# Kernel optimization log

Measured on AMD Instinct MI355X. Metric: run time of the kernel, lower is better.

Reference implementation:

```python
import jax, jax.numpy as jnp
import numpy as np
from jax import lax

D_MODEL = 1024
LN_EPS = 1e-5


def setup_inputs() -> dict:
    key = jax.random.key(0)
    ks = jax.random.split(key, 9)
    B, L, D = 2, 2048, D_MODEL
    x = jax.random.normal(ks[0], (B, L, D), dtype=jnp.float32)
    A_param = jax.random.normal(ks[1], (D,), dtype=jnp.float32) * 0.1
    B_vec = jax.random.normal(ks[2], (D,), dtype=jnp.float32)
    C_vec = jax.random.normal(ks[3], (D,), dtype=jnp.float32)
    D_vec = jax.random.normal(ks[4], (D,), dtype=jnp.float32)
    # nn.Linear(d, d): weight (D, D) applied as x @ W.T + b
    W_proj = jax.random.normal(ks[5], (D, D), dtype=jnp.float32) * (1.0 / np.sqrt(D))
    b_proj = jax.random.normal(ks[6], (D,), dtype=jnp.float32) * 0.01
    gamma = jnp.ones((D,), dtype=jnp.float32)
    beta = jnp.zeros((D,), dtype=jnp.float32)
    return {"x": x, "A_param": A_param, "B_vec": B_vec, "C_vec": C_vec,
            "D_vec": D_vec, "W_proj": W_proj, "b_proj": b_proj,
            "gamma": gamma, "beta": beta}


def _layer_norm(x, gamma, beta):
    mu = jnp.mean(x, axis=-1, keepdims=True)
    var = jnp.mean(jnp.square(x - mu), axis=-1, keepdims=True)
    return (x - mu) * lax.rsqrt(var + LN_EPS) * gamma + beta


def reference(x, A_param, B_vec, C_vec, D_vec, W_proj, b_proj, gamma, beta):
    Bsz, L, D = x.shape
    A = jax.nn.sigmoid(A_param)                      # (D,)
    t = jnp.arange(L, dtype=jnp.float32)             # (L,)
    A_t = A[:, None] ** t[None, :]                   # (D, L) geometric decay
    K = (C_vec[:, None] * A_t * B_vec[:, None])[:, None, :]  # (D, 1, L)
    x_t = jnp.transpose(x, (0, 2, 1))                # (B, D, L)
    # depthwise cross-correlation with padding L-1 on both sides (matches torch F.conv1d)
    out = lax.conv_general_dilated(
        x_t, K, window_strides=(1,), padding=[(L - 1, L - 1)],
        dimension_numbers=("NCH", "OIH", "NCH"), feature_group_count=D)
    out = out[..., :L] + D_vec[None, :, None] * x_t  # (B, D, L)
    out = jnp.transpose(out, (0, 2, 1))              # (B, L, D)
    out = jnp.dot(jax.nn.gelu(out, approximate=False), W_proj.T) + b_proj
    return _layer_norm(x + out, gamma, beta)
```

## Files before the change

### kernel.cpp

```cpp
#include <hip/hip_runtime.h>
#include <hip/hip_bf16.h>
#include <math.h>

#define D_MODEL 1024
#define LSEQ 2048
#define BATCH 2
#define NROWS (BATCH*LSEQ)
#define NACT 8
#define CHSL 32

typedef __bf16 bf16;
typedef __attribute__((ext_vector_type(8))) __bf16 bf16x8;
typedef __attribute__((ext_vector_type(4))) __bf16 bf16x4;
typedef __attribute__((ext_vector_type(4))) float f32x4;

__device__ __forceinline__ float sigA(float ap) {
    return fmaxf(1.0f / (1.0f + expf(-ap)), 1e-30f);
}

__device__ __forceinline__ void gload_lds16(const void* g, void* l) {
    __builtin_amdgcn_global_load_lds(
        (const __attribute__((address_space(1))) void*)g,
        (__attribute__((address_space(3))) void*)l, 16, 0, 0);
}

__global__ __launch_bounds__(256) void k_misc(const float* __restrict__ W, bf16* __restrict__ Wb,
                                              const float* __restrict__ x,
                                              const float* __restrict__ A_param,
                                              float* __restrict__ partial) {
    if (blockIdx.x < 1024) {
        int idx = (blockIdx.x * 256 + threadIdx.x) * 4;
        f32x4 v = *reinterpret_cast<const f32x4*>(W + idx);
        bf16x4 o;
        #pragma unroll
        for (int k = 0; k < 4; ++k) o[k] = (bf16)v[k];
        *reinterpret_cast<bf16x4*>(Wb + idx) = o;
        return;
    }
    const int flat = blockIdx.x - 1024;
    const int c = flat & 7, dg = (flat >> 3) & 3, b = flat >> 5;
    const int d = dg * 256 + threadIdx.x;
    const float A = sigA(A_param[d]);
    const float l2A = log2f(A);
    const int s0 = c * CHSL;
    float w = exp2f((float)s0 * l2A);
    float sum = 0.0f;
    const int jmax = (c == NACT - 1) ? (LSEQ - s0) : CHSL;
    if (w != 0.0f) {
        const float* xp = x + ((size_t)b * LSEQ + s0) * D_MODEL + d;
        for (int j0 = 0; j0 < jmax; j0 += 8) {
            if (w == 0.0f) break;
            #pragma unroll
            for (int j = 0; j < 8; ++j) {
                sum += w * xp[(size_t)(j0 + j) * D_MODEL];
                w *= A;
            }
        }
    }
    partial[((size_t)b * NACT + c) * D_MODEL + d] = sum;
}

__global__ __launch_bounds__(256) void k_prep(const float* __restrict__ x,
                                              const float* __restrict__ A_param,
                                              const float* __restrict__ Bv,
                                              const float* __restrict__ Cv,
                                              const float* __restrict__ Dv,
                                              const float* __restrict__ partial,
                                              bf16* __restrict__ G) {
    const int ib = blockIdx.x, b = blockIdx.z;
    const int i0 = ib * 8;
    const int d0 = threadIdx.x * 4;
    f32x4 P = {0.f, 0.f, 0.f, 0.f};
    #pragma unroll
    for (int c = 0; c < NACT; ++c)
        P += *reinterpret_cast<const f32x4*>(partial + ((size_t)b * NACT + c) * D_MODEL + d0);
    float A4[4], coeff[4], dvv[4], w[4];
    #pragma unroll
    for (int k = 0; k < 4; ++k) {
        A4[k] = sigA(A_param[d0 + k]);
        float l2 = log2f(A4[k]);
        coeff[k] = Cv[d0 + k] * Bv[d0 + k] * P[k];
        dvv[k] = Dv[d0 + k];
        w[k] = exp2f((float)(LSEQ - 1 - (i0 + 7)) * l2);
    }
    for (int j = 7; j >= 0; --j) {
        const int i = i0 + j;
        f32x4 xv = *reinterpret_cast<const f32x4*>(x + ((size_t)b * LSEQ + i) * D_MODEL + d0);
        bf16x4 g;
        #pragma unroll
        for (int k = 0; k < 4; ++k) {
            float u = coeff[k] * w[k] + dvv[k] * xv[k];
            g[k] = (bf16)(0.5f * u * (1.0f + erff(u * 0.70710678118654752f)));
            w[k] *= A4[k];
        }
        *reinterpret_cast<bf16x4*>(G + ((size_t)b * LSEQ + i) * D_MODEL + d0) = g;
    }
}

__global__ __launch_bounds__(256) void k_gemm(const bf16* __restrict__ G,
                                              const bf16* __restrict__ Wb,
                                              const float* __restrict__ bias,
                                              bf16* __restrict__ Z) {
    __shared__ __align__(16) bf16 S[3 * 12288];
    const int tid = threadIdx.x;
    const int lane = tid & 63, wave = tid >> 6;
    const int bid = blockIdx.x;
    const int bx = (bid & 7) * 8 + ((bid >> 3) & 7);
    const int by = bid >> 6;
    const int row0 = bx * 64, col0 = by * 128;
    const int wr = wave >> 1, wc = wave & 1;
    const int fr = lane & 15, q = lane >> 4;
    const int fx = fr & 7;
    f32x4 acc[2][4] = {};

    const int lr8 = lane >> 3;
    const int sb = 16 * ((lane & 7) ^ lr8);
    const bf16* srcbase[6];
    #pragma unroll
    for (int r = 0; r < 6; ++r) {
        const int c = wave * 6 + r;
        const bf16* mat;
        int row;
        if (c < 8) { mat = G;  row = row0 + c * 8 + lr8; }
        else       { mat = Wb; row = col0 + (c - 8) * 8 + lr8; }
        srcbase[r] = (const bf16*)((const char*)(mat + (size_t)row * D_MODEL) + sb);
    }

    auto stage = [&](int buf, int k0) {
        #pragma unroll
        for (int r = 0; r < 6; ++r)
            gload_lds16(srcbase[r] + k0, &S[buf * 12288 + (wave * 6 + r) * 512]);
    };

    stage(0, 0);
    stage(1, 64);
    for (int t = 0; t < 16; ++t) {
        const int cur = t % 3;
        if (t + 2 < 16) stage((t + 2) % 3, (t + 2) * 64);
        __builtin_amdgcn_sched_barrier(0);
        if (t < 14)       asm volatile("s_waitcnt vmcnt(12)" ::: "memory");
        else if (t == 14) asm volatile("s_waitcnt vmcnt(6)"  ::: "memory");
        else              asm volatile("s_waitcnt vmcnt(0)"  ::: "memory");
        __builtin_amdgcn_s_barrier();
        __builtin_amdgcn_sched_barrier(0);
        const bf16* SA = &S[cur * 12288];
        const bf16* SB = SA + 4096;
        bf16x8 a[2][2], bb[4][2];
        #pragma unroll
        for (int fm = 0; fm < 2; ++fm)
            #pragma unroll
            for (int ks = 0; ks < 2; ++ks)
                a[fm][ks] = *reinterpret_cast<const bf16x8*>(
                    SA + (wr * 32 + fm * 16 + fr) * 64 + 8 * ((4 * ks + q) ^ fx));
        #pragma unroll
        for (int fn = 0; fn < 4; ++fn)
            #pragma unroll
            for (int ks = 0; ks < 2; ++ks)
                bb[fn][ks] = *reinterpret_cast<const bf16x8*>(
                    SB + (wc * 64 + fn * 16 + fr) * 64 + 8 * ((4 * ks + q) ^ fx));
        #pragma unroll
        for (int fm = 0; fm < 2; ++fm)
            #pragma unroll
            for (int fn = 0; fn < 4; ++fn)
                #pragma unroll
                for (int ks = 0; ks < 2; ++ks)
                    acc[fm][fn] = __builtin_amdgcn_mfma_f32_16x16x32_bf16(a[fm][ks], bb[fn][ks], acc[fm][fn], 0, 0, 0);
        __builtin_amdgcn_sched_barrier(0);
        __builtin_amdgcn_s_barrier();
    }
    #pragma unroll
    for (int fm = 0; fm < 2; ++fm) {
        const int rbase = row0 + wr * 32 + fm * 16 + (lane >> 4) * 4;
        #pragma unroll
        for (int fn = 0; fn < 4; ++fn) {
            const int c = col0 + wc * 64 + fn * 16 + fr;
            const float bv = bias[c];
            #pragma unroll
            for (int r = 0; r < 4; ++r)
                Z[(size_t)(rbase + r) * D_MODEL + c] = (bf16)(acc[fm][fn][r] + bv);
        }
    }
}

__global__ __launch_bounds__(256) void k_ln(const bf16* __restrict__ Z,
                                            const float* __restrict__ x,
                                            const float* __restrict__ gamma,
                                            const float* __restrict__ beta,
                                            float* __restrict__ out) {
    const int row = blockIdx.x;
    const int t = threadIdx.x;
    bf16x4 zv = *reinterpret_cast<const bf16x4*>(Z + (size_t)row * D_MODEL + t * 4);
    f32x4 xv = *reinterpret_cast<const f32x4*>(x + (size_t)row * D_MODEL + t * 4);
    float z[4];
    float s = 0.0f, sq = 0.0f;
    #pragma unroll
    for (int k = 0; k < 4; ++k) {
        z[k] = xv[k] + (float)zv[k];
        s += z[k]; sq += z[k] * z[k];
    }
    #pragma unroll
    for (int o = 1; o < 64; o <<= 1) { s += __shfl_xor(s, o, 64); sq += __shfl_xor(sq, o, 64); }
    __shared__ float ls[4], lq[4];
    const int wave = t >> 6;
    if ((t & 63) == 0) { ls[wave] = s; lq[wave] = sq; }
    __syncthreads();
    s = ls[0] + ls[1] + ls[2] + ls[3];
    sq = lq[0] + lq[1] + lq[2] + lq[3];
    const float mu = s * (1.0f / D_MODEL);
    const float var = sq * (1.0f / D_MODEL) - mu * mu;
    const float inv = rsqrtf(var + 1e-5f);
    f32x4 g = *reinterpret_cast<const f32x4*>(gamma + t * 4);
    f32x4 be = *reinterpret_cast<const f32x4*>(beta + t * 4);
    f32x4 o;
    #pragma unroll
    for (int k = 0; k < 4; ++k) o[k] = (z[k] - mu) * inv * g[k] + be[k];
    *reinterpret_cast<f32x4*>(out + (size_t)row * D_MODEL + t * 4) = o;
}

extern "C" void kernel_launch(void* const* d_in, const int* in_sizes, int n_in,
                              void* d_out, int out_size, void* d_ws, size_t ws_size,
                              hipStream_t stream) {
    const float* x       = (const float*)d_in[0];
    const float* A_param = (const float*)d_in[1];
    const float* B_vec   = (const float*)d_in[2];
    const float* C_vec   = (const float*)d_in[3];
    const float* D_vec   = (const float*)d_in[4];
    const float* W       = (const float*)d_in[5];
    const float* b_proj  = (const float*)d_in[6];
    const float* gamma   = (const float*)d_in[7];
    const float* beta    = (const float*)d_in[8];
    float* out = (float*)d_out;

    char* ws = (char*)d_ws;
    float* partial = (float*)ws;
    bf16*  Wb      = (bf16*)(ws + (128 << 10));
    bf16*  G       = (bf16*)(ws + (128 << 10) + (2 << 20));
    bf16*  Z       = (bf16*)(ws + (128 << 10) + (10 << 20));

    hipLaunchKernelGGL(k_misc, dim3(1088), dim3(256), 0, stream, W, Wb, x, A_param, partial);
    hipLaunchKernelGGL(k_prep, dim3(LSEQ / 8, 1, BATCH), dim3(256), 0, stream,
                       x, A_param, B_vec, C_vec, D_vec, partial, G);
    hipLaunchKernelGGL(k_gemm, dim3(512), dim3(256), 0, stream, G, Wb, b_proj, Z);
    hipLaunchKernelGGL(k_ln,   dim3(NROWS), dim3(256), 0, stream, Z, x, gamma, beta, out);
}
```

Measured before the change: 41.30 us.

## Double-buffer GEMM register fragments and overlap LDS reads with MFMA

Result: no change. 41.06 us (-0.6%).

```diff
diff --git a/kernel.cpp b/kernel.cpp
--- a/kernel.cpp
+++ b/kernel.cpp
@@ -132,20 +132,11 @@
             gload_lds16(srcbase[r] + k0, &S[buf * 12288 + (wave * 6 + r) * 512]);
     };
 
-    stage(0, 0);
-    stage(1, 64);
-    for (int t = 0; t < 16; ++t) {
-        const int cur = t % 3;
-        if (t + 2 < 16) stage((t + 2) % 3, (t + 2) * 64);
-        __builtin_amdgcn_sched_barrier(0);
-        if (t < 14)       asm volatile("s_waitcnt vmcnt(12)" ::: "memory");
-        else if (t == 14) asm volatile("s_waitcnt vmcnt(6)"  ::: "memory");
-        else              asm volatile("s_waitcnt vmcnt(0)"  ::: "memory");
-        __builtin_amdgcn_s_barrier();
-        __builtin_amdgcn_sched_barrier(0);
-        const bf16* SA = &S[cur * 12288];
+    bf16x8 aE[2][2], bE[4][2], aO[2][2], bO[4][2];
+
+    auto readFrags = [&](int bufI, bf16x8 (&a)[2][2], bf16x8 (&bb)[4][2]) {
+        const bf16* SA = &S[bufI * 12288];
         const bf16* SB = SA + 4096;
-        bf16x8 a[2][2], bb[4][2];
         #pragma unroll
         for (int fm = 0; fm < 2; ++fm)
             #pragma unroll
@@ -158,6 +149,10 @@
             for (int ks = 0; ks < 2; ++ks)
                 bb[fn][ks] = *reinterpret_cast<const bf16x8*>(
                     SB + (wc * 64 + fn * 16 + fr) * 64 + 8 * ((4 * ks + q) ^ fx));
+    };
+
+    auto mfmaAll = [&](bf16x8 (&a)[2][2], bf16x8 (&bb)[4][2]) {
+        __builtin_amdgcn_s_setprio(1);
         #pragma unroll
         for (int fm = 0; fm < 2; ++fm)
             #pragma unroll
@@ -165,9 +160,37 @@
                 #pragma unroll
                 for (int ks = 0; ks < 2; ++ks)
                     acc[fm][fn] = __builtin_amdgcn_mfma_f32_16x16x32_bf16(a[fm][ks], bb[fn][ks], acc[fm][fn], 0, 0, 0);
-        __builtin_amdgcn_sched_barrier(0);
-        __builtin_amdgcn_s_barrier();
-    }
+        __builtin_amdgcn_s_setprio(0);
+    };
+
+    stage(0, 0);
+    stage(1, 64);
+    asm volatile("s_waitcnt vmcnt(6)" ::: "memory");
+    __builtin_amdgcn_s_barrier();
+    __builtin_amdgcn_sched_barrier(0);
+    readFrags(0, aE, bE);
+
+    #define ITER_BODY(T, ACUR, BCUR, ANXT, BNXT)                                   \
+    {                                                                              \
+        if ((T) + 2 < 16) stage(((T) + 2) % 3, ((T) + 2) * 64);                    \
+        __builtin_amdgcn_sched_barrier(0);                                         \
+        asm volatile("s_waitcnt lgkmcnt(0)" ::: "memory");                         \
+        if ((T) + 2 < 16)      asm volatile("s_waitcnt vmcnt(6)" ::: "memory");    \
+        else if ((T) + 1 < 16) asm volatile("s_waitcnt vmcnt(0)" ::: "memory");    \
+        __builtin_amdgcn_sched_barrier(0);                                         \
+        __builtin_amdgcn_s_barrier();                                              \
+        __builtin_amdgcn_sched_barrier(0);                                         \
+        if ((T) + 1 < 16) readFrags(((T) + 1) % 3, ANXT, BNXT);                    \
+        mfmaAll(ACUR, BCUR);                                                       \
+    }
+
+    #pragma unroll
+    for (int tt = 0; tt < 16; tt += 2) {
+        ITER_BODY(tt, aE, bE, aO, bO);
+        ITER_BODY(tt + 1, aO, bO, aE, bE);
+    }
+    #undef ITER_BODY
+
     #pragma unroll
     for (int fm = 0; fm < 2; ++fm) {
         const int rbase = row0 + wr * 32 + fm * 16 + (lane >> 4) * 4;
```
